# Kernel tuning notes

Hardware: AMD Instinct MI355X
Metric: run time of the kernel (lower is better)

## Reference

```python
import jax, jax.numpy as jnp
import numpy as np

S_CNT, R_CNT, P_CNT = 10000, 10000, 50000
K_S, K_R, K_P = 64, 64, 128
T = 50
N = 1_000_000


def setup_inputs() -> dict:
    key = jax.random.key(0)
    ks, kr, kp, kt, kws, kwr, kwp = jax.random.split(key, 7)
    s = jax.random.randint(ks, (N,), 0, S_CNT)
    r = jax.random.randint(kr, (N,), 0, R_CNT)
    p = jax.random.randint(kp, (N,), 0, P_CNT)
    t = jax.random.randint(kt, (N,), 0, T)
    X = jnp.stack([s, r, p, t], axis=1).astype(jnp.int64)  # n x 4
    # xavier_uniform-like init: bound = sqrt(6/(fan_in+fan_out))
    def xavier(k, shape):
        bound = np.sqrt(6.0 / (shape[0] + shape[1])).astype(np.float32)
        return jax.random.uniform(k, shape, jnp.float32, -bound, bound)
    s_embeds = xavier(kws, (T * S_CNT, K_S))
    r_embeds = xavier(kwr, (T * R_CNT, K_R))
    p_embeds = xavier(kwp, (P_CNT, K_P))
    return {"X": X, "s_embeds": s_embeds, "r_embeds": r_embeds, "p_embeds": p_embeds}


def reference(X, s_embeds, r_embeds, p_embeds):
    s, r, p, t = X[:, 0], X[:, 1], X[:, 2], X[:, 3]
    st = s + t * S_CNT
    rt = r + t * R_CNT
    se = s_embeds[st]            # [n, K_S]
    re = r_embeds[rt]            # [n, K_R]
    pe = p_embeds[p]             # [n, K_S + K_R]
    # dot(concat(se, re), pe) without materializing the concat
    prod = jnp.sum(se * pe[:, :K_S], axis=1) + jnp.sum(re * pe[:, K_S:], axis=1)
    return jax.nn.sigmoid(prod)  # [n]
```

## Files before the change

### kernel.cpp

```cpp
#include <hip/hip_runtime.h>
#include <cstdint>

#define S_CNT 10000
#define R_CNT 10000
#define PG 1024
#define PROWS 49
#define CAP 1216
#define SPLIT 2
#define PACKED_OFF_B 16384
#define WS_NEED ((size_t)PACKED_OFF_B + 8ull * PG * CAP)

__device__ __forceinline__ unsigned bfpack(float a, float b) {
    unsigned ua = __float_as_uint(a), ub = __float_as_uint(b);
    ua = (ua + 0x7FFFu + ((ua >> 16) & 1u)) >> 16;
    ub = (ub + 0x7FFFu + ((ub >> 16) & 1u)) >> 16;
    return ua | (ub << 16);
}
__device__ __forceinline__ float blo(unsigned u) { return __uint_as_float(u << 16); }
__device__ __forceinline__ float bhi(unsigned u) { return __uint_as_float(u & 0xFFFF0000u); }

__global__ __launch_bounds__(256) void zero_kernel(int4* __restrict__ cur4) {
    cur4[threadIdx.x] = make_int4(0, 0, 0, 0);
}

__global__ __launch_bounds__(256) void bin_kernel(
    const int* __restrict__ X, int n, int* __restrict__ cursors,
    int2* __restrict__ packed,
    const float* __restrict__ se, const float* __restrict__ re,
    const float* __restrict__ pe, float* __restrict__ out)
{
    __shared__ int lhist[PG], lbase[PG], lcur[PG];
    const int tid = threadIdx.x;
    const long long base = (long long)blockIdx.x * 1024;

    #pragma unroll
    for (int k = 0; k < PG / 256; ++k) lhist[tid + 256 * k] = 0;
    __syncthreads();

    int4 xs[4];
    int  grp[4];
    #pragma unroll
    for (int it = 0; it < 4; ++it) {
        const long long i = base + it * 256 + tid;
        if (i < n) {
            xs[it] = *reinterpret_cast<const int4*>(X + 4 * i);
            grp[it] = xs[it].z / PROWS;
            atomicAdd(&lhist[grp[it]], 1);
        } else grp[it] = -1;
    }
    __syncthreads();
    #pragma unroll
    for (int k = 0; k < PG / 256; ++k) {
        const int b = tid + 256 * k;
        const int c = lhist[b];
        lbase[b] = c ? atomicAdd(&cursors[b], c) : 0;
        lcur[b] = 0;
    }
    __syncthreads();
    #pragma unroll
    for (int it = 0; it < 4; ++it) {
        const int g = grp[it];
        if (g < 0) continue;
        const unsigned i = (unsigned)(base + it * 256 + tid);
        const int rank = lbase[g] + atomicAdd(&lcur[g], 1);
        if (rank < CAP) {
            const unsigned dp = (unsigned)(xs[it].z - g * PROWS);
            packed[g * CAP + rank] = make_int2(
                (int)((unsigned)xs[it].x | ((unsigned)xs[it].w << 14) | (dp << 20) | ((i & 63u) << 26)),
                (int)((unsigned)xs[it].y | ((i >> 6) << 14)));
        } else {
            const long long st = (long long)xs[it].x + (long long)xs[it].w * S_CNT;
            const long long rt = (long long)xs[it].y + (long long)xs[it].w * R_CNT;
            const long long p  = xs[it].z;
            float acc = 0.f;
            for (int k = 0; k < 64; ++k)
                acc += se[st * 64 + k] * pe[p * 128 + k]
                     + re[rt * 64 + k] * pe[p * 128 + 64 + k];
            out[i] = 1.0f / (1.0f + __expf(-acc));
        }
    }
}

__global__ __launch_bounds__(256, 8) void compute_kernel(
    const int* __restrict__ cursors, const int2* __restrict__ packed,
    const float* __restrict__ s_embeds, const float* __restrict__ r_embeds,
    const float* __restrict__ p_embeds, float* __restrict__ out)
{
    __shared__ __align__(16) unsigned plds[PROWS * 64];
    const int g = blockIdx.x / SPLIT;
    const int q = blockIdx.x % SPLIT;
    const int cnt = min(cursors[g], CAP);
    if (cnt == 0) return;

    const int prow0 = g * PROWS;
    const int rows = min(PROWS, 50000 - prow0);
    const int nf4 = rows * 32;
    const float4* src = reinterpret_cast<const float4*>(p_embeds + (long long)prow0 * 128);
    for (int k = threadIdx.x; k < nf4; k += 256) {
        const float4 v = src[k];
        uint2 u;
        u.x = bfpack(v.x, v.y);
        u.y = bfpack(v.z, v.w);
        reinterpret_cast<uint2*>(plds)[k] = u;
    }
    __syncthreads();

    const int mid = (cnt / 2) & ~63;
    const int lo  = (q == 0) ? 0 : mid;
    const int end = (q == 0) ? mid : cnt;
    if (lo >= end) return;

    const int gl = threadIdx.x >> 4;
    const int l  = threadIdx.x & 15;
    const int2* pk = packed + g * CAP;

    for (int sb = lo; sb < end; sb += 64) {
        const int j0 = sb + gl * 4;
        int2 rec[4];
        if (j0 + 3 < end) {
            const int4 w01 = *reinterpret_cast<const int4*>(pk + j0);
            const int4 w23 = *reinterpret_cast<const int4*>(pk + j0 + 2);
            rec[0] = make_int2(w01.x, w01.y); rec[1] = make_int2(w01.z, w01.w);
            rec[2] = make_int2(w23.x, w23.y); rec[3] = make_int2(w23.z, w23.w);
        } else {
            #pragma unroll
            for (int k = 0; k < 4; ++k) rec[k] = pk[min(j0 + k, end - 1)];
        }

        int st[4], rt[4], dp[4], idx[4];
        #pragma unroll
        for (int k = 0; k < 4; ++k) {
            const unsigned w0 = (unsigned)rec[k].x, w1 = (unsigned)rec[k].y;
            const int s = w0 & 0x3FFF;
            const int t = (w0 >> 14) & 0x3F;
            dp[k]  = (w0 >> 20) & 0x3F;
            idx[k] = (int)((w0 >> 26) | ((w1 >> 14) << 6));
            const int r = w1 & 0x3FFF;
            st[k] = s + t * S_CNT;
            rt[k] = r + t * R_CNT;
        }

        float4 se[4], re[4];
        #pragma unroll
        for (int k = 0; k < 4; ++k)
            se[k] = *reinterpret_cast<const float4*>(s_embeds + (unsigned)st[k] * 64u + l * 4);
        #pragma unroll
        for (int k = 0; k < 4; ++k)
            re[k] = *reinterpret_cast<const float4*>(r_embeds + (unsigned)rt[k] * 64u + l * 4);

        float acc[4];
        #pragma unroll
        for (int k = 0; k < 4; ++k) {
            const int pb = dp[k] * 64;
            const uint2 upl = *reinterpret_cast<const uint2*>(&plds[pb + l * 2]);
            const uint2 uph = *reinterpret_cast<const uint2*>(&plds[pb + 32 + l * 2]);
            acc[k] = se[k].x * blo(upl.x) + se[k].y * bhi(upl.x)
                   + se[k].z * blo(upl.y) + se[k].w * bhi(upl.y)
                   + re[k].x * blo(uph.x) + re[k].y * bhi(uph.x)
                   + re[k].z * blo(uph.y) + re[k].w * bhi(uph.y);
        }

        #pragma unroll
        for (int k = 0; k < 4; ++k) {
            acc[k] += __shfl_xor(acc[k], 1, 64);
            acc[k] += __shfl_xor(acc[k], 2, 64);
            acc[k] += __shfl_xor(acc[k], 4, 64);
            acc[k] += __shfl_xor(acc[k], 8, 64);
        }

        if (l == 0) {
            #pragma unroll
            for (int k = 0; k < 4; ++k)
                if (j0 + k < end) out[idx[k]] = 1.0f / (1.0f + __expf(-acc[k]));
        }
    }
}

__global__ __launch_bounds__(256) void direct_kernel(
    const int* __restrict__ X,
    const float* __restrict__ s_embeds, const float* __restrict__ r_embeds,
    const float* __restrict__ p_embeds, float* __restrict__ out, int n) {
    const int g = threadIdx.x >> 4;
    const int l = threadIdx.x & 15;
    const int i = blockIdx.x * 16 + g;
    if (i >= n) return;
    const int4 xi = *reinterpret_cast<const int4*>(X + 4ll * i);
    const long long st = (long long)xi.x + (long long)xi.w * S_CNT;
    const long long rt = (long long)xi.y + (long long)xi.w * R_CNT;
    const long long p  = xi.z;
    const float4 se = *reinterpret_cast<const float4*>(s_embeds + st * 64 + l * 4);
    const float4 re = *reinterpret_cast<const float4*>(r_embeds + rt * 64 + l * 4);
    const float4 pl = *reinterpret_cast<const float4*>(p_embeds + p * 128 + l * 4);
    const float4 ph = *reinterpret_cast<const float4*>(p_embeds + p * 128 + 64 + l * 4);
    float acc = se.x * pl.x + se.y * pl.y + se.z * pl.z + se.w * pl.w
              + re.x * ph.x + re.y * ph.y + re.z * ph.z + re.w * ph.w;
    acc += __shfl_xor(acc, 1, 64);
    acc += __shfl_xor(acc, 2, 64);
    acc += __shfl_xor(acc, 4, 64);
    acc += __shfl_xor(acc, 8, 64);
    if (l == 0) out[i] = 1.0f / (1.0f + __expf(-acc));
}

extern "C" void kernel_launch(void* const* d_in, const int* in_sizes, int n_in,
                              void* d_out, int out_size, void* d_ws, size_t ws_size,
                              hipStream_t stream) {
    const int*   X        = (const int*)d_in[0];
    const float* s_embeds = (const float*)d_in[1];
    const float* r_embeds = (const float*)d_in[2];
    const float* p_embeds = (const float*)d_in[3];
    float* out = (float*)d_out;
    const int n = in_sizes[0] / 4;

    if (ws_size < WS_NEED) {
        direct_kernel<<<(n + 15) / 16, 256, 0, stream>>>(
            X, s_embeds, r_embeds, p_embeds, out, n);
        return;
    }

    int* cursors = (int*)d_ws;
    int2* packed = reinterpret_cast<int2*>((char*)d_ws + PACKED_OFF_B);

    zero_kernel<<<1, 256, 0, stream>>>(reinterpret_cast<int4*>(cursors));
    bin_kernel<<<(n + 1023) / 1024, 256, 0, stream>>>(
        X, n, cursors, packed, s_embeds, r_embeds, p_embeds, out);
    compute_kernel<<<PG * SPLIT, 256, 0, stream>>>(
        cursors, packed, s_embeds, r_embeds, p_embeds, out);
}
```

Measured before the change: 143.4 us.

## Software-pipeline compute kernel gathers with double-buffered two-record stages

Restructures the compute kernel's loop so that each 16-lane group handles two records per step and prefetches the next step's packed records and s/r embedding rows into a second register set while computing the current one. This is meant to hide gather latency behind the dot-product and shuffle reduction instead of issuing all loads and then waiting. Indices are clamped so speculative loads past the end stay in bounds. The split point between the two blocks changes to 32-record granularity, and the occupancy hint drops from 8 to 7 waves to leave room for the extra registers.

```diff
diff --git a/kernel.cpp b/kernel.cpp
--- a/kernel.cpp
+++ b/kernel.cpp
@@ -9,6 +9,7 @@
 #define SPLIT 2
 #define PACKED_OFF_B 16384
 #define WS_NEED ((size_t)PACKED_OFF_B + 8ull * PG * CAP)
+#define MAXROW (S_CNT * 50 - 1)
 
 __device__ __forceinline__ unsigned bfpack(float a, float b) {
     unsigned ua = __float_as_uint(a), ub = __float_as_uint(b);
@@ -81,7 +82,54 @@
     }
 }
 
-__global__ __launch_bounds__(256, 8) void compute_kernel(
+#define PIPE_LOAD(S, jv)                                                        \
+    {                                                                           \
+        jA_##S = (jv);                                                          \
+        const int jc = min(jA_##S, CAP - 2);                                    \
+        const int4 w = *reinterpret_cast<const int4*>(pk + jc);                 \
+        const unsigned a0 = (unsigned)w.x, a1 = (unsigned)w.y;                  \
+        const unsigned b0 = (unsigned)w.z, b1 = (unsigned)w.w;                  \
+        const int stA = min((int)(a0 & 0x3FFFu) + (int)((a0 >> 14) & 0x3Fu) * S_CNT, MAXROW); \
+        const int rtA = min((int)(a1 & 0x3FFFu) + (int)((a0 >> 14) & 0x3Fu) * R_CNT, MAXROW); \
+        const int stB = min((int)(b0 & 0x3FFFu) + (int)((b0 >> 14) & 0x3Fu) * S_CNT, MAXROW); \
+        const int rtB = min((int)(b1 & 0x3FFFu) + (int)((b0 >> 14) & 0x3Fu) * R_CNT, MAXROW); \
+        dpA_##S  = min((int)((a0 >> 20) & 0x3Fu), PROWS - 1);                   \
+        idxA_##S = (int)((a0 >> 26) | ((a1 >> 14) << 6));                       \
+        dpB_##S  = min((int)((b0 >> 20) & 0x3Fu), PROWS - 1);                   \
+        idxB_##S = (int)((b0 >> 26) | ((b1 >> 14) << 6));                       \
+        seA_##S = *reinterpret_cast<const float4*>(sbase + (unsigned)stA * 64u);\
+        reA_##S = *reinterpret_cast<const float4*>(rbase + (unsigned)rtA * 64u);\
+        seB_##S = *reinterpret_cast<const float4*>(sbase + (unsigned)stB * 64u);\
+        reB_##S = *reinterpret_cast<const float4*>(rbase + (unsigned)rtB * 64u);\
+    }
+
+#define PIPE_COMPUTE(S)                                                         \
+    {                                                                           \
+        const int pbA = dpA_##S * 64;                                           \
+        const int pbB = dpB_##S * 64;                                           \
+        const uint2 uplA = *reinterpret_cast<const uint2*>(&plds[pbA + l * 2]); \
+        const uint2 uphA = *reinterpret_cast<const uint2*>(&plds[pbA + 32 + l * 2]); \
+        const uint2 uplB = *reinterpret_cast<const uint2*>(&plds[pbB + l * 2]); \
+        const uint2 uphB = *reinterpret_cast<const uint2*>(&plds[pbB + 32 + l * 2]); \
+        float accA = seA_##S.x * blo(uplA.x) + seA_##S.y * bhi(uplA.x)          \
+                   + seA_##S.z * blo(uplA.y) + seA_##S.w * bhi(uplA.y)          \
+                   + reA_##S.x * blo(uphA.x) + reA_##S.y * bhi(uphA.x)          \
+                   + reA_##S.z * blo(uphA.y) + reA_##S.w * bhi(uphA.y);         \
+        float accB = seB_##S.x * blo(uplB.x) + seB_##S.y * bhi(uplB.x)          \
+                   + seB_##S.z * blo(uplB.y) + seB_##S.w * bhi(uplB.y)          \
+                   + reB_##S.x * blo(uphB.x) + reB_##S.y * bhi(uphB.x)          \
+                   + reB_##S.z * blo(uphB.y) + reB_##S.w * bhi(uphB.y);         \
+        accA += __shfl_xor(accA, 1, 64);  accB += __shfl_xor(accB, 1, 64);      \
+        accA += __shfl_xor(accA, 2, 64);  accB += __shfl_xor(accB, 2, 64);      \
+        accA += __shfl_xor(accA, 4, 64);  accB += __shfl_xor(accB, 4, 64);      \
+        accA += __shfl_xor(accA, 8, 64);  accB += __shfl_xor(accB, 8, 64);      \
+        if (l == 0) {                                                           \
+            if (jA_##S     <= last) out[idxA_##S] = 1.0f / (1.0f + __expf(-accA)); \
+            if (jA_##S + 1 <= last) out[idxB_##S] = 1.0f / (1.0f + __expf(-accB)); \
+        }                                                                       \
+    }
+
+__global__ __launch_bounds__(256, 7) void compute_kernel(
     const int* __restrict__ cursors, const int2* __restrict__ packed,
     const float* __restrict__ s_embeds, const float* __restrict__ r_embeds,
     const float* __restrict__ p_embeds, float* __restrict__ out)
@@ -105,73 +153,37 @@
     }
     __syncthreads();
 
-    const int mid = (cnt / 2) & ~63;
-    const int lo  = (q == 0) ? 0 : mid;
-    const int end = (q == 0) ? mid : cnt;
+    int mid = (cnt / 2 + 31) & ~31;
+    if (mid > cnt) mid = cnt;
+    const int lo  = q ? mid : 0;
+    const int end = q ? cnt : mid;
     if (lo >= end) return;
+    const int last = end - 1;
 
     const int gl = threadIdx.x >> 4;
     const int l  = threadIdx.x & 15;
     const int2* pk = packed + g * CAP;
-
-    for (int sb = lo; sb < end; sb += 64) {
-        const int j0 = sb + gl * 4;
-        int2 rec[4];
-        if (j0 + 3 < end) {
-            const int4 w01 = *reinterpret_cast<const int4*>(pk + j0);
-            const int4 w23 = *reinterpret_cast<const int4*>(pk + j0 + 2);
-            rec[0] = make_int2(w01.x, w01.y); rec[1] = make_int2(w01.z, w01.w);
-            rec[2] = make_int2(w23.x, w23.y); rec[3] = make_int2(w23.z, w23.w);
-        } else {
-            #pragma unroll
-            for (int k = 0; k < 4; ++k) rec[k] = pk[min(j0 + k, end - 1)];
-        }
-
-        int st[4], rt[4], dp[4], idx[4];
-        #pragma unroll
-        for (int k = 0; k < 4; ++k) {
-            const unsigned w0 = (unsigned)rec[k].x, w1 = (unsigned)rec[k].y;
-            const int s = w0 & 0x3FFF;
-            const int t = (w0 >> 14) & 0x3F;
-            dp[k]  = (w0 >> 20) & 0x3F;
-            idx[k] = (int)((w0 >> 26) | ((w1 >> 14) << 6));
-            const int r = w1 & 0x3FFF;
-            st[k] = s + t * S_CNT;
-            rt[k] = r + t * R_CNT;
-        }
-
-        float4 se[4], re[4];
-        #pragma unroll
-        for (int k = 0; k < 4; ++k)
-            se[k] = *reinterpret_cast<const float4*>(s_embeds + (unsigned)st[k] * 64u + l * 4);
-        #pragma unroll
-        for (int k = 0; k < 4; ++k)
-            re[k] = *reinterpret_cast<const float4*>(r_embeds + (unsigned)rt[k] * 64u + l * 4);
-
-        float acc[4];
-        #pragma unroll
-        for (int k = 0; k < 4; ++k) {
-            const int pb = dp[k] * 64;
-            const uint2 upl = *reinterpret_cast<const uint2*>(&plds[pb + l * 2]);
-            const uint2 uph = *reinterpret_cast<const uint2*>(&plds[pb + 32 + l * 2]);
-            acc[k] = se[k].x * blo(upl.x) + se[k].y * bhi(upl.x)
-                   + se[k].z * blo(upl.y) + se[k].w * bhi(upl.y)
-                   + re[k].x * blo(uph.x) + re[k].y * bhi(uph.x)
-                   + re[k].z * blo(uph.y) + re[k].w * bhi(uph.y);
-        }
-
-        #pragma unroll
-        for (int k = 0; k < 4; ++k) {
-            acc[k] += __shfl_xor(acc[k], 1, 64);
-            acc[k] += __shfl_xor(acc[k], 2, 64);
-            acc[k] += __shfl_xor(acc[k], 4, 64);
-            acc[k] += __shfl_xor(acc[k], 8, 64);
-        }
-
-        if (l == 0) {
-            #pragma unroll
-            for (int k = 0; k < 4; ++k)
-                if (j0 + k < end) out[idx[k]] = 1.0f / (1.0f + __expf(-acc[k]));
+    const float* sbase = s_embeds + l * 4;
+    const float* rbase = r_embeds + l * 4;
+
+    int jA_0, dpA_0, idxA_0, dpB_0, idxB_0;
+    int jA_1, dpA_1, idxA_1, dpB_1, idxB_1;
+    float4 seA_0, reA_0, seB_0, reB_0;
+    float4 seA_1, reA_1, seB_1, reB_1;
+
+    int j = lo + gl * 2;
+    if (j <= last) {
+        PIPE_LOAD(0, j);
+        j += 32;
+        while (true) {
+            if (j > last) { PIPE_COMPUTE(0); break; }
+            PIPE_LOAD(1, j);
+            PIPE_COMPUTE(0);
+            j += 32;
+            if (j > last) { PIPE_COMPUTE(1); break; }
+            PIPE_LOAD(0, j);
+            PIPE_COMPUTE(1);
+            j += 32;
         }
     }
 }
```

Result: slower. 179.6 us (+25.2%).
